# Optimization experiments

Measured on AMD Instinct MI355X. Metric: run time of the kernel, lower is better.

The kernel has to match this reference:

```python
import jax, jax.numpy as jnp
import numpy as np

LN_EPS = 1e-5  # torch nn.LayerNorm default


def layernorm(x, g, b):
    mu = jnp.mean(x, axis=-1, keepdims=True)
    var = jnp.var(x, axis=-1, keepdims=True)
    return (x - mu) * jax.lax.rsqrt(var + LN_EPS) * g + b


def setup_inputs() -> dict:
    key = jax.random.key(0)
    ks = jax.random.split(key, 12)
    B, N, Dn, Dm, E, L = 4, 20000, 64, 128, 160000, 2
    inp = {}
    inp["node_feat"] = jax.random.normal(ks[0], (B, N, Dn), jnp.float32)
    inp["in_W"] = jax.random.normal(ks[1], (Dn, Dm), jnp.float32) * 0.1
    inp["in_b"] = jnp.zeros((Dm,), jnp.float32)
    inp["node_W"] = jax.random.normal(ks[2], (L, 3, Dm, Dm), jnp.float32) * 0.05
    inp["node_b"] = jnp.zeros((L, 3, Dm), jnp.float32)
    inp["edge_W"] = jax.random.normal(ks[3], (L, 2, 16, Dm), jnp.float32) * 0.1
    inp["edge_b"] = jnp.zeros((L, 2, Dm), jnp.float32)
    inp["ln_g"] = jnp.ones((L, Dm), jnp.float32)
    inp["ln_b"] = jnp.zeros((L, Dm), jnp.float32)
    inp["ea0"] = jax.random.normal(ks[4], (E, 16), jnp.float32)
    inp["ea1"] = jax.random.normal(ks[5], (E, 16), jnp.float32)
    inp["ei0"] = jax.random.randint(ks[6], (2, E), 0, N)
    inp["ei1"] = jax.random.randint(ks[7], (2, E), 0, N)
    inp["ei2"] = jax.random.randint(ks[8], (2, E), 0, N)
    return inp


def reference(node_feat, in_W, in_b, node_W, node_b, edge_W, edge_b, ln_g, ln_b,
              ea0, ea1, ei0, ei1, ei2):
    # input projection: [B,N,Dn] -> [B,N,Dm]
    H = node_feat @ in_W + in_b
    edge_idx = [ei0, ei1, ei2]
    edge_attr = [ea0, ea1, None]  # relation 2 has edge_attr_dims == 0 (Identity/skip)
    n_layers = node_W.shape[0]
    for l in range(n_layers):
        agg = jnp.zeros_like(H)
        for r in range(3):
            src, dst = edge_idx[r][0], edge_idx[r][1]
            # gather src nodes per batch then per-relation linear: [B,E,Dm]
            msg = H[:, src] @ node_W[l, r] + node_b[l, r]
            if edge_attr[r] is not None:
                # edge attrs shared across batch -> broadcast add
                msg = msg + (edge_attr[r] @ edge_W[l, r] + edge_b[l, r])[None]
            # scatter-add messages to dst nodes, batched
            agg = agg.at[:, dst].add(msg)
        H = layernorm(H + jax.nn.relu(agg), ln_g[l], ln_b[l])
    return H
```

## Files before the change

### kernel.cpp

```cpp
#include <hip/hip_runtime.h>


#define NNODES 20000
#define NB     4
#define BROWS  (NB * NNODES)
#define DN     64
#define DM     128
#define NE     160000
#define CAP    64
#define LN_EPS 1e-5f
#define KE     448
#define LDW    88
#define HTW    132
#define FOW    132
#define UOW    136

typedef __attribute__((ext_vector_type(8))) short bf16x8;
typedef __attribute__((ext_vector_type(4))) float f32x4;

__device__ inline float bf2f(unsigned short u) {
    union { unsigned int i; float f; } x; x.i = ((unsigned int)u) << 16; return x.f;
}
__device__ inline unsigned short f2bf(float f) {
    union { float f; unsigned int i; } x; x.f = f;
    unsigned int r = x.i + 0x7FFFu + ((x.i >> 16) & 1u);
    return (unsigned short)(r >> 16);
}

__global__ void k_scatter(const int* __restrict__ ei0, const int* __restrict__ ei1,
                          const int* __restrict__ ei2, int* __restrict__ cursor,
                          int* __restrict__ srcs, int* __restrict__ eids) {
    int tid = blockIdx.x * blockDim.x + threadIdx.x;
    if (tid >= 3 * NE) return;
    int r = tid / NE, e = tid - r * NE;
    const int* ei = (r == 0) ? ei0 : ((r == 1) ? ei1 : ei2);
    int src = ei[e], dst = ei[NE + e];
    int p = atomicAdd(&cursor[r * NNODES + dst], 1);
    if (p < CAP) {
        srcs[(r * NNODES + dst) * CAP + p] = src;
        if (r < 2) eids[(r * NNODES + dst) * CAP + p] = e;
    }
}

__global__ __launch_bounds__(256) void k_sgather(const int* __restrict__ deg,
                                                 const int* __restrict__ eids,
                                                 const float* __restrict__ ea0,
                                                 const float* __restrict__ ea1,
                                                 float* __restrict__ S) {
    int task = blockIdx.x * 4 + (threadIdx.x >> 6);
    int r = task / NNODES;
    const float* ea = r ? ea1 : ea0;
    int lane = threadIdx.x & 63;
    int k = lane & 15, sub = lane >> 4;
    int dg = deg[task]; if (dg > CAP) dg = CAP;
    const int* bk = eids + (size_t)task * CAP;
    float acc = 0.f;
    for (int j = sub; j < dg; j += 4) {
        int e = bk[j];
        acc += ea[e * 16 + k];
    }
    acc += __shfl_xor(acc, 16, 64);
    acc += __shfl_xor(acc, 32, 64);
    if (lane < 16) S[(size_t)task * 16 + k] = acc;
}

__global__ __launch_bounds__(256) void k_wprep(const float* __restrict__ nW,
                                               const float* __restrict__ nb,
                                               const float* __restrict__ eW,
                                               const float* __restrict__ eb,
                                               const float* __restrict__ inW,
                                               unsigned short* __restrict__ Wt,
                                               unsigned short* __restrict__ Wp) {
    int lin = blockIdx.x * 256 + threadIdx.x;
    if (lin < 2 * 128 * KE) {
        int l = lin / (128 * KE);
        int rem = lin - l * 128 * KE;
        int n = rem / KE, k = rem - n * KE;
        float v;
        if (k < 384) {
            int r = k >> 7, kk = k & 127;
            v = nW[(((size_t)(l * 3 + r) * 128) + kk) * 128 + n];
        } else {
            int e = k - 384;
            if (e < 3) {
                v = nb[(l * 3 + e) * DM + n];
                if (e < 2) v += eb[(l * 2 + e) * DM + n];
            } else if (e < 35) {
                int r2 = (e - 3) >> 4, j = (e - 3) & 15;
                v = eW[((size_t)((l * 2 + r2) * 16 + j)) * DM + n];
            } else v = 0.f;
        }
        Wt[lin] = f2bf(v);
    } else {
        int i = lin - 2 * 128 * KE;
        int n = i >> 6, k = i & 63;
        Wp[n * 64 + k] = f2bf(inW[(size_t)k * DM + n]);
    }
}

__global__ __launch_bounds__(256) void k_proj(const float* __restrict__ X,
                                              const unsigned short* __restrict__ Wp,
                                              const float* __restrict__ bias,
                                              unsigned short* __restrict__ HB) {
    __shared__ __align__(16) unsigned char smem[33792];
    unsigned short* As = (unsigned short*)smem;
    unsigned short* Bs = (unsigned short*)(smem + 11264);
    unsigned short* UO = (unsigned short*)smem;
    int t = threadIdx.x;
    int m0 = blockIdx.x * 64;
#pragma unroll
    for (int i = 0; i < 4; ++i) {
        int lin = t + 256 * i;
        int row = lin >> 4, seg = lin & 15;
        float4 v = *(const float4*)(X + (size_t)(m0 + row) * DN + seg * 4);
        ushort4 h; h.x = f2bf(v.x); h.y = f2bf(v.y); h.z = f2bf(v.z); h.w = f2bf(v.w);
        *(ushort4*)&As[row * LDW + seg * 4] = h;
    }
#pragma unroll
    for (int i = 0; i < 4; ++i) {
        int lin = t + 256 * i;
        int row = lin >> 3, seg = lin & 7;
        *(uint4*)&Bs[row * LDW + seg * 8] = *(const uint4*)(Wp + (size_t)row * 64 + seg * 8);
    }
    __syncthreads();
    int w = t >> 6, lane = t & 63;
    int q = lane >> 4, lm = lane & 15;
    f32x4 acc[8];
#pragma unroll
    for (int ct = 0; ct < 8; ++ct) acc[ct] = (f32x4){0.f, 0.f, 0.f, 0.f};
#pragma unroll
    for (int kt = 0; kt < 2; ++kt) {
        bf16x8 a = *(const bf16x8*)&As[(w * 16 + lm) * LDW + kt * 32 + q * 8];
#pragma unroll
        for (int ct = 0; ct < 8; ++ct) {
            bf16x8 bf = *(const bf16x8*)&Bs[(ct * 16 + lm) * LDW + kt * 32 + q * 8];
            acc[ct] = __builtin_amdgcn_mfma_f32_16x16x32_bf16(a, bf, acc[ct], 0, 0, 0);
        }
    }
    __syncthreads();
#pragma unroll
    for (int reg = 0; reg < 4; ++reg) {
        int rl = w * 16 + q * 4 + reg;
#pragma unroll
        for (int ct = 0; ct < 8; ++ct) {
            int col = ct * 16 + lm;
            UO[rl * UOW + col] = f2bf(acc[ct][reg] + bias[col]);
        }
    }
    __syncthreads();
#pragma unroll
    for (int i = 0; i < 4; ++i) {
        int lin = t + 256 * i;
        int row = lin >> 4, seg = lin & 15;
        *(uint4*)(HB + (size_t)(m0 + row) * DM + seg * 8) = *(uint4*)&UO[row * UOW + seg * 8];
    }
}

__global__ __launch_bounds__(256) void k_spmm(const unsigned short* __restrict__ HB,
                                              const int* __restrict__ deg,
                                              const int* __restrict__ srcs,
                                              const float* __restrict__ S,
                                              unsigned short* __restrict__ G) {
    int blk = blockIdx.x;
    int s = blk & 7;
    int bb = s >> 1;
    int idx = ((blk >> 3) << 1) + (s & 1);
    int n0 = idx * 16;
    int g = threadIdx.x >> 4, lane = threadIdx.x & 15;
    int n = n0 + g;
    int c8 = lane * 8;
    const unsigned short* Hb = HB + (size_t)bb * NNODES * DM;
    size_t rowbase = ((size_t)(bb * NNODES + n)) * KE;
    int dt[3];
#pragma unroll
    for (int r = 0; r < 3; ++r) {
        dt[r] = deg[r * NNODES + n];
        int dg = dt[r] > CAP ? CAP : dt[r];
        const int* bk = srcs + (size_t)(r * NNODES + n) * CAP;
        float a[8];
#pragma unroll
        for (int j = 0; j < 8; ++j) a[j] = 0.f;
        int j = 0;
        for (; j + 3 < dg; j += 4) {
            int4 s4 = *(const int4*)&bk[j];
            ushort4 u0 = *(const ushort4*)(Hb + (size_t)s4.x * DM + c8);
            ushort4 u1 = *(const ushort4*)(Hb + (size_t)s4.x * DM + c8 + 4);
            ushort4 v0 = *(const ushort4*)(Hb + (size_t)s4.y * DM + c8);
            ushort4 v1 = *(const ushort4*)(Hb + (size_t)s4.y * DM + c8 + 4);
            ushort4 w0 = *(const ushort4*)(Hb + (size_t)s4.z * DM + c8);
            ushort4 w1 = *(const ushort4*)(Hb + (size_t)s4.z * DM + c8 + 4);
            ushort4 x0 = *(const ushort4*)(Hb + (size_t)s4.w * DM + c8);
            ushort4 x1 = *(const ushort4*)(Hb + (size_t)s4.w * DM + c8 + 4);
            a[0] += bf2f(u0.x) + bf2f(v0.x) + bf2f(w0.x) + bf2f(x0.x);
            a[1] += bf2f(u0.y) + bf2f(v0.y) + bf2f(w0.y) + bf2f(x0.y);
            a[2] += bf2f(u0.z) + bf2f(v0.z) + bf2f(w0.z) + bf2f(x0.z);
            a[3] += bf2f(u0.w) + bf2f(v0.w) + bf2f(w0.w) + bf2f(x0.w);
            a[4] += bf2f(u1.x) + bf2f(v1.x) + bf2f(w1.x) + bf2f(x1.x);
            a[5] += bf2f(u1.y) + bf2f(v1.y) + bf2f(w1.y) + bf2f(x1.y);
            a[6] += bf2f(u1.z) + bf2f(v1.z) + bf2f(w1.z) + bf2f(x1.z);
            a[7] += bf2f(u1.w) + bf2f(v1.w) + bf2f(w1.w) + bf2f(x1.w);
        }
        for (; j < dg; ++j) {
            int s0 = bk[j];
            ushort4 u0 = *(const ushort4*)(Hb + (size_t)s0 * DM + c8);
            ushort4 u1 = *(const ushort4*)(Hb + (size_t)s0 * DM + c8 + 4);
            a[0] += bf2f(u0.x); a[1] += bf2f(u0.y); a[2] += bf2f(u0.z); a[3] += bf2f(u0.w);
            a[4] += bf2f(u1.x); a[5] += bf2f(u1.y); a[6] += bf2f(u1.z); a[7] += bf2f(u1.w);
        }
        ushort4 o0, o1;
        o0.x = f2bf(a[0]); o0.y = f2bf(a[1]); o0.z = f2bf(a[2]); o0.w = f2bf(a[3]);
        o1.x = f2bf(a[4]); o1.y = f2bf(a[5]); o1.z = f2bf(a[6]); o1.w = f2bf(a[7]);
        *(ushort4*)(G + rowbase + r * 128 + c8) = o0;
        *(ushort4*)(G + rowbase + r * 128 + c8 + 4) = o1;
    }
    if (lane < 8) {
        ushort4 e0, e1;
        unsigned short ev[8];
#pragma unroll
        for (int j = 0; j < 8; ++j) {
            int kk = lane * 8 + j;
            float v;
            if (kk < 3)       v = (float)dt[kk];
            else if (kk < 19) v = S[((size_t)(0 * NNODES + n)) * 16 + (kk - 3)];
            else if (kk < 35) v = S[((size_t)(1 * NNODES + n)) * 16 + (kk - 19)];
            else              v = 0.f;
            ev[j] = f2bf(v);
        }
        e0.x = ev[0]; e0.y = ev[1]; e0.z = ev[2]; e0.w = ev[3];
        e1.x = ev[4]; e1.y = ev[5]; e1.z = ev[6]; e1.w = ev[7];
        *(ushort4*)(G + rowbase + 384 + lane * 8) = e0;
        *(ushort4*)(G + rowbase + 384 + lane * 8 + 4) = e1;
    }
}

__global__ __launch_bounds__(256) void k_gemm_ln(const unsigned short* __restrict__ G,
                                                 const unsigned short* __restrict__ Wt,
                                                 unsigned short* HB,
                                                 const float* __restrict__ lng,
                                                 const float* __restrict__ lnb,
                                                 float* __restrict__ out, int write_f32) {
    __shared__ __align__(16) unsigned char smem[50688];
    unsigned short* Gs = (unsigned short*)smem;
    unsigned short* Ws = (unsigned short*)(smem + 11264);
    unsigned short* HT = (unsigned short*)smem;
    float*          FO = (float*)(smem + 16896);
    unsigned short* UO = (unsigned short*)(smem + 16896);
    int t = threadIdx.x;
    int m0 = blockIdx.x * 64;
    int w = t >> 6, lane = t & 63;
    int q = lane >> 4, lm = lane & 15;

    f32x4 acc[8];
#pragma unroll
    for (int ct = 0; ct < 8; ++ct) acc[ct] = (f32x4){0.f, 0.f, 0.f, 0.f};

    for (int kc = 0; kc < 7; ++kc) {
#pragma unroll
        for (int i = 0; i < 2; ++i) {
            int lin = t + 256 * i;
            int row = lin >> 3, seg = lin & 7;
            *(uint4*)&Gs[row * LDW + seg * 8] =
                *(const uint4*)(G + (size_t)(m0 + row) * KE + kc * 64 + seg * 8);
        }
#pragma unroll
        for (int i = 0; i < 4; ++i) {
            int lin = t + 256 * i;
            int row = lin >> 3, seg = lin & 7;
            *(uint4*)&Ws[row * LDW + seg * 8] =
                *(const uint4*)(Wt + (size_t)row * KE + kc * 64 + seg * 8);
        }
        __syncthreads();
#pragma unroll
        for (int kt = 0; kt < 2; ++kt) {
            bf16x8 a = *(const bf16x8*)&Gs[(w * 16 + lm) * LDW + kt * 32 + q * 8];
#pragma unroll
            for (int ct = 0; ct < 8; ++ct) {
                bf16x8 bf = *(const bf16x8*)&Ws[(ct * 16 + lm) * LDW + kt * 32 + q * 8];
                acc[ct] = __builtin_amdgcn_mfma_f32_16x16x32_bf16(a, bf, acc[ct], 0, 0, 0);
            }
        }
        __syncthreads();
    }

#pragma unroll
    for (int i = 0; i < 4; ++i) {
        int lin = t + 256 * i;
        int row = lin >> 4, seg = lin & 15;
        *(uint4*)&HT[row * HTW + seg * 8] = *(const uint4*)(HB + (size_t)(m0 + row) * DM + seg * 8);
    }
    __syncthreads();

    float gc[8], bc[8];
#pragma unroll
    for (int ct = 0; ct < 8; ++ct) {
        int col = ct * 16 + lm;
        gc[ct] = lng[col]; bc[ct] = lnb[col];
    }
#pragma unroll
    for (int reg = 0; reg < 4; ++reg) {
        int rl = w * 16 + q * 4 + reg;
        float xv[8];
        float s1 = 0.f, s2 = 0.f;
#pragma unroll
        for (int ct = 0; ct < 8; ++ct) {
            int col = ct * 16 + lm;
            float h = bf2f(HT[rl * HTW + col]);
            float v = h + fmaxf(acc[ct][reg], 0.f);
            xv[ct] = v; s1 += v; s2 += v * v;
        }
#pragma unroll
        for (int m = 1; m <= 8; m <<= 1) {
            s1 += __shfl_xor(s1, m, 64);
            s2 += __shfl_xor(s2, m, 64);
        }
        float mu  = s1 * (1.f / 128.f);
        float var = s2 * (1.f / 128.f) - mu * mu;
        float inv = rsqrtf(var + LN_EPS);
        if (write_f32) {
#pragma unroll
            for (int ct = 0; ct < 8; ++ct) {
                int col = ct * 16 + lm;
                FO[rl * FOW + col] = (xv[ct] - mu) * inv * gc[ct] + bc[ct];
            }
        } else {
#pragma unroll
            for (int ct = 0; ct < 8; ++ct) {
                int col = ct * 16 + lm;
                UO[rl * UOW + col] = f2bf((xv[ct] - mu) * inv * gc[ct] + bc[ct]);
            }
        }
    }
    __syncthreads();
    if (write_f32) {
#pragma unroll
        for (int i = 0; i < 8; ++i) {
            int lin = t + 256 * i;
            int row = lin >> 5, seg = lin & 31;
            *(float4*)(out + (size_t)(m0 + row) * DM + seg * 4) = *(float4*)&FO[row * FOW + seg * 4];
        }
    } else {
#pragma unroll
        for (int i = 0; i < 4; ++i) {
            int lin = t + 256 * i;
            int row = lin >> 4, seg = lin & 15;
            *(uint4*)(HB + (size_t)(m0 + row) * DM + seg * 8) = *(uint4*)&UO[row * UOW + seg * 8];
        }
    }
}

extern "C" void kernel_launch(void* const* d_in, const int* in_sizes, int n_in,
                              void* d_out, int out_size, void* d_ws, size_t ws_size,
                              hipStream_t stream) {
    const float* node_feat = (const float*)d_in[0];
    const float* in_W   = (const float*)d_in[1];
    const float* in_b   = (const float*)d_in[2];
    const float* node_W = (const float*)d_in[3];
    const float* node_b = (const float*)d_in[4];
    const float* edge_W = (const float*)d_in[5];
    const float* edge_b = (const float*)d_in[6];
    const float* ln_g   = (const float*)d_in[7];
    const float* ln_b   = (const float*)d_in[8];
    const float* ea0    = (const float*)d_in[9];
    const float* ea1    = (const float*)d_in[10];
    const int*   ei0    = (const int*)d_in[11];
    const int*   ei1    = (const int*)d_in[12];
    const int*   ei2    = (const int*)d_in[13];
    float* out = (float*)d_out;

    char* ws = (char*)d_ws;
    size_t off = 0;
    auto alloc = [&](size_t bytes) -> void* {
        void* p = ws + off;
        off = (off + bytes + 255) & ~(size_t)255;
        return p;
    };
    unsigned short* HB     = (unsigned short*)alloc((size_t)BROWS * DM * 2);
    unsigned short* G      = (unsigned short*)alloc((size_t)BROWS * KE * 2);
    int*            cursor = (int*)alloc((size_t)3 * NNODES * 4);
    float*          S      = (float*)alloc((size_t)2 * NNODES * 16 * 4);
    int*            srcs   = (int*)alloc((size_t)3 * NNODES * CAP * 4);
    int*            eids   = (int*)alloc((size_t)2 * NNODES * CAP * 4);
    unsigned short* Wt     = (unsigned short*)alloc((size_t)2 * 128 * KE * 2);
    unsigned short* Wp     = (unsigned short*)alloc((size_t)128 * 64 * 2);

    hipMemsetAsync(cursor, 0, (size_t)3 * NNODES * 4, stream);

    k_scatter<<<(3 * NE + 255) / 256, 256, 0, stream>>>(ei0, ei1, ei2, cursor, srcs, eids);
    k_sgather<<<(2 * NNODES) / 4, 256, 0, stream>>>(cursor, eids, ea0, ea1, S);
    k_wprep<<<480, 256, 0, stream>>>(node_W, node_b, edge_W, edge_b, in_W, Wt, Wp);
    k_proj<<<BROWS / 64, 256, 0, stream>>>(node_feat, Wp, in_b, HB);

    for (int l = 0; l < 2; ++l) {
        k_spmm<<<5000, 256, 0, stream>>>(HB, cursor, srcs, S, G);
        k_gemm_ln<<<BROWS / 64, 256, 0, stream>>>(G, Wt + (size_t)l * 128 * KE, HB,
                                                  ln_g + (size_t)l * DM, ln_b + (size_t)l * DM,
                                                  out, l == 1);
    }
}
```

Baseline: 332.7 us.

## Widen spmm gathers to 16B per lane, add nontemporal hints, drop LDS H staging

The SpMM gather now assigns 8 lanes per node-half, so each lane loads a full 16-byte chunk of a source row instead of two 8-byte loads. Blocks split the feature dimension into halves across adjacent block indices. Index loads and G reads/writes use nontemporal hints so the streaming G buffer does not pollute the cache. The gemm+LN kernel stops staging the residual H tile in LDS and reads it straight from global memory, which cuts shared memory use and may raise occupancy, at the cost of strided uncoalesced global reads.

Result: slower. 451.8 us (+35.8%).

```diff
diff --git a/kernel.cpp b/kernel.cpp
--- a/kernel.cpp
+++ b/kernel.cpp
@@ -11,12 +11,13 @@
 #define LN_EPS 1e-5f
 #define KE     448
 #define LDW    88
-#define HTW    132
 #define FOW    132
 #define UOW    136
 
 typedef __attribute__((ext_vector_type(8))) short bf16x8;
 typedef __attribute__((ext_vector_type(4))) float f32x4;
+typedef __attribute__((ext_vector_type(4))) unsigned int u32x4;
+typedef __attribute__((ext_vector_type(4))) int i32x4;
 
 __device__ inline float bf2f(unsigned short u) {
     union { unsigned int i; float f; } x; x.i = ((unsigned int)u) << 16; return x.f;
@@ -25,6 +26,12 @@
     union { float f; unsigned int i; } x; x.f = f;
     unsigned int r = x.i + 0x7FFFu + ((x.i >> 16) & 1u);
     return (unsigned short)(r >> 16);
+}
+__device__ inline float lo16f(unsigned int u) {
+    union { unsigned int i; float f; } x; x.i = u << 16; return x.f;
+}
+__device__ inline float hi16f(unsigned int u) {
+    union { unsigned int i; float f; } x; x.i = u & 0xFFFF0000u; return x.f;
 }
 
 __global__ void k_scatter(const int* __restrict__ ei0, const int* __restrict__ ei1,
@@ -163,12 +170,11 @@
                                               unsigned short* __restrict__ G) {
     int blk = blockIdx.x;
     int s = blk & 7;
-    int bb = s >> 1;
-    int idx = ((blk >> 3) << 1) + (s & 1);
-    int n0 = idx * 16;
-    int g = threadIdx.x >> 4, lane = threadIdx.x & 15;
-    int n = n0 + g;
-    int c8 = lane * 8;
+    int bb = s >> 1, half = s & 1;
+    int idx = blk >> 3;
+    int n = idx * 32 + (threadIdx.x >> 3);
+    int lane8 = threadIdx.x & 7;
+    int cb = half * 64 + lane8 * 8;
     const unsigned short* Hb = HB + (size_t)bb * NNODES * DM;
     size_t rowbase = ((size_t)(bb * NNODES + n)) * KE;
     int dt[3];
@@ -182,43 +188,40 @@
         for (int j = 0; j < 8; ++j) a[j] = 0.f;
         int j = 0;
         for (; j + 3 < dg; j += 4) {
-            int4 s4 = *(const int4*)&bk[j];
-            ushort4 u0 = *(const ushort4*)(Hb + (size_t)s4.x * DM + c8);
-            ushort4 u1 = *(const ushort4*)(Hb + (size_t)s4.x * DM + c8 + 4);
-            ushort4 v0 = *(const ushort4*)(Hb + (size_t)s4.y * DM + c8);
-            ushort4 v1 = *(const ushort4*)(Hb + (size_t)s4.y * DM + c8 + 4);
-            ushort4 w0 = *(const ushort4*)(Hb + (size_t)s4.z * DM + c8);
-            ushort4 w1 = *(const ushort4*)(Hb + (size_t)s4.z * DM + c8 + 4);
-            ushort4 x0 = *(const ushort4*)(Hb + (size_t)s4.w * DM + c8);
-            ushort4 x1 = *(const ushort4*)(Hb + (size_t)s4.w * DM + c8 + 4);
-            a[0] += bf2f(u0.x) + bf2f(v0.x) + bf2f(w0.x) + bf2f(x0.x);
-            a[1] += bf2f(u0.y) + bf2f(v0.y) + bf2f(w0.y) + bf2f(x0.y);
-            a[2] += bf2f(u0.z) + bf2f(v0.z) + bf2f(w0.z) + bf2f(x0.z);
-            a[3] += bf2f(u0.w) + bf2f(v0.w) + bf2f(w0.w) + bf2f(x0.w);
-            a[4] += bf2f(u1.x) + bf2f(v1.x) + bf2f(w1.x) + bf2f(x1.x);
-            a[5] += bf2f(u1.y) + bf2f(v1.y) + bf2f(w1.y) + bf2f(x1.y);
-            a[6] += bf2f(u1.z) + bf2f(v1.z) + bf2f(w1.z) + bf2f(x1.z);
-            a[7] += bf2f(u1.w) + bf2f(v1.w) + bf2f(w1.w) + bf2f(x1.w);
+            i32x4 s4 = __builtin_nontemporal_load((const i32x4*)&bk[j]);
+            u32x4 v0 = *(const u32x4*)(Hb + (size_t)s4.x * DM + cb);
+            u32x4 v1 = *(const u32x4*)(Hb + (size_t)s4.y * DM + cb);
+            u32x4 v2 = *(const u32x4*)(Hb + (size_t)s4.z * DM + cb);
+            u32x4 v3 = *(const u32x4*)(Hb + (size_t)s4.w * DM + cb);
+            a[0] += lo16f(v0.x) + lo16f(v1.x) + lo16f(v2.x) + lo16f(v3.x);
+            a[1] += hi16f(v0.x) + hi16f(v1.x) + hi16f(v2.x) + hi16f(v3.x);
+            a[2] += lo16f(v0.y) + lo16f(v1.y) + lo16f(v2.y) + lo16f(v3.y);
+            a[3] += hi16f(v0.y) + hi16f(v1.y) + hi16f(v2.y) + hi16f(v3.y);
+            a[4] += lo16f(v0.z) + lo16f(v1.z) + lo16f(v2.z) + lo16f(v3.z);
+            a[5] += hi16f(v0.z) + hi16f(v1.z) + hi16f(v2.z) + hi16f(v3.z);
+            a[6] += lo16f(v0.w) + lo16f(v1.w) + lo16f(v2.w) + lo16f(v3.w);
+            a[7] += hi16f(v0.w) + hi16f(v1.w) + hi16f(v2.w) + hi16f(v3.w);
         }
         for (; j < dg; ++j) {
             int s0 = bk[j];
-            ushort4 u0 = *(const ushort4*)(Hb + (size_t)s0 * DM + c8);
-            ushort4 u1 = *(const ushort4*)(Hb + (size_t)s0 * DM + c8 + 4);
-            a[0] += bf2f(u0.x); a[1] += bf2f(u0.y); a[2] += bf2f(u0.z); a[3] += bf2f(u0.w);
-            a[4] += bf2f(u1.x); a[5] += bf2f(u1.y); a[6] += bf2f(u1.z); a[7] += bf2f(u1.w);
-        }
-        ushort4 o0, o1;
-        o0.x = f2bf(a[0]); o0.y = f2bf(a[1]); o0.z = f2bf(a[2]); o0.w = f2bf(a[3]);
-        o1.x = f2bf(a[4]); o1.y = f2bf(a[5]); o1.z = f2bf(a[6]); o1.w = f2bf(a[7]);
-        *(ushort4*)(G + rowbase + r * 128 + c8) = o0;
-        *(ushort4*)(G + rowbase + r * 128 + c8 + 4) = o1;
-    }
-    if (lane < 8) {
-        ushort4 e0, e1;
+            u32x4 v0 = *(const u32x4*)(Hb + (size_t)s0 * DM + cb);
+            a[0] += lo16f(v0.x); a[1] += hi16f(v0.x);
+            a[2] += lo16f(v0.y); a[3] += hi16f(v0.y);
+            a[4] += lo16f(v0.z); a[5] += hi16f(v0.z);
+            a[6] += lo16f(v0.w); a[7] += hi16f(v0.w);
+        }
+        u32x4 o;
+        o.x = (unsigned int)f2bf(a[0]) | ((unsigned int)f2bf(a[1]) << 16);
+        o.y = (unsigned int)f2bf(a[2]) | ((unsigned int)f2bf(a[3]) << 16);
+        o.z = (unsigned int)f2bf(a[4]) | ((unsigned int)f2bf(a[5]) << 16);
+        o.w = (unsigned int)f2bf(a[6]) | ((unsigned int)f2bf(a[7]) << 16);
+        __builtin_nontemporal_store(o, (u32x4*)(G + rowbase + r * 128 + cb));
+    }
+    if (lane8 < 4) {
         unsigned short ev[8];
 #pragma unroll
         for (int j = 0; j < 8; ++j) {
-            int kk = lane * 8 + j;
+            int kk = half * 32 + lane8 * 8 + j;
             float v;
             if (kk < 3)       v = (float)dt[kk];
             else if (kk < 19) v = S[((size_t)(0 * NNODES + n)) * 16 + (kk - 3)];
@@ -226,10 +229,12 @@
             else              v = 0.f;
             ev[j] = f2bf(v);
         }
-        e0.x = ev[0]; e0.y = ev[1]; e0.z = ev[2]; e0.w = ev[3];
-        e1.x = ev[4]; e1.y = ev[5]; e1.z = ev[6]; e1.w = ev[7];
-        *(ushort4*)(G + rowbase + 384 + lane * 8) = e0;
-        *(ushort4*)(G + rowbase + 384 + lane * 8 + 4) = e1;
+        u32x4 o;
+        o.x = (unsigned int)ev[0] | ((unsigned int)ev[1] << 16);
+        o.y = (unsigned int)ev[2] | ((unsigned int)ev[3] << 16);
+        o.z = (unsigned int)ev[4] | ((unsigned int)ev[5] << 16);
+        o.w = (unsigned int)ev[6] | ((unsigned int)ev[7] << 16);
+        __builtin_nontemporal_store(o, (u32x4*)(G + rowbase + 384 + half * 32 + lane8 * 8));
     }
 }
 
@@ -239,12 +244,11 @@
                                                  const float* __restrict__ lng,
                                                  const float* __restrict__ lnb,
                                                  float* __restrict__ out, int write_f32) {
-    __shared__ __align__(16) unsigned char smem[50688];
+    __shared__ __align__(16) unsigned char smem[33792];
     unsigned short* Gs = (unsigned short*)smem;
     unsigned short* Ws = (unsigned short*)(smem + 11264);
-    unsigned short* HT = (unsigned short*)smem;
-    float*          FO = (float*)(smem + 16896);
-    unsigned short* UO = (unsigned short*)(smem + 16896);
+    float*          FO = (float*)smem;
+    unsigned short* UO = (unsigned short*)smem;
     int t = threadIdx.x;
     int m0 = blockIdx.x * 64;
     int w = t >> 6, lane = t & 63;
@@ -259,8 +263,9 @@
         for (int i = 0; i < 2; ++i) {
             int lin = t + 256 * i;
             int row = lin >> 3, seg = lin & 7;
-            *(uint4*)&Gs[row * LDW + seg * 8] =
-                *(const uint4*)(G + (size_t)(m0 + row) * KE + kc * 64 + seg * 8);
+            u32x4 v = __builtin_nontemporal_load(
+                (const u32x4*)(G + (size_t)(m0 + row) * KE + kc * 64 + seg * 8));
+            *(u32x4*)&Gs[row * LDW + seg * 8] = v;
         }
 #pragma unroll
         for (int i = 0; i < 4; ++i) {
@@ -282,14 +287,6 @@
         __syncthreads();
     }
 
-#pragma unroll
-    for (int i = 0; i < 4; ++i) {
-        int lin = t + 256 * i;
-        int row = lin >> 4, seg = lin & 15;
-        *(uint4*)&HT[row * HTW + seg * 8] = *(const uint4*)(HB + (size_t)(m0 + row) * DM + seg * 8);
-    }
-    __syncthreads();
-
     float gc[8], bc[8];
 #pragma unroll
     for (int ct = 0; ct < 8; ++ct) {
@@ -299,12 +296,13 @@
 #pragma unroll
     for (int reg = 0; reg < 4; ++reg) {
         int rl = w * 16 + q * 4 + reg;
+        size_t row = (size_t)m0 + rl;
         float xv[8];
         float s1 = 0.f, s2 = 0.f;
 #pragma unroll
         for (int ct = 0; ct < 8; ++ct) {
             int col = ct * 16 + lm;
-            float h = bf2f(HT[rl * HTW + col]);
+            float h = bf2f(HB[row * DM + col]);
             float v = h + fmaxf(acc[ct][reg], 0.f);
             xv[ct] = v; s1 += v; s2 += v * v;
         }
@@ -383,7 +381,7 @@
     unsigned short* Wt     = (unsigned short*)alloc((size_t)2 * 128 * KE * 2);
     unsigned short* Wp     = (unsigned short*)alloc((size_t)128 * 64 * 2);
 
-    hipMemsetAsync(cursor, 0, (size_t)3 * NNODES * 4, stream);
+    (void)hipMemsetAsync(cursor, 0, (size_t)3 * NNODES * 4, stream);
 
     k_scatter<<<(3 * NE + 255) / 256, 256, 0, stream>>>(ei0, ei1, ei2, cursor, srcs, eids);
     k_sgather<<<(2 * NNODES) / 4, 256, 0, stream>>>(cursor, eids, ea0, ea1, S);
```
